# Performance work log

Measured on AMD Instinct MI355X. Metric: run time of the kernel, lower is better.

## Reference

```python
import jax, jax.numpy as jnp
import numpy as np
import math

B, N_SEQ, SEQ_LEN, C_M = 1, 256, 256, 256
N_HEADS, C_HIDDEN = 8, 32
HC = N_HEADS * C_HIDDEN
LN_EPS = 1e-5


def setup_inputs() -> dict:
    key = jax.random.key(0)
    ks = jax.random.split(key, 8)
    s_in = 1.0 / math.sqrt(C_M)
    s_out = 1.0 / math.sqrt(HC)
    return {
        "m": jax.random.normal(ks[0], (B, N_SEQ, SEQ_LEN, C_M), dtype=jnp.float32),
        "ln_w": jnp.ones((C_M,), dtype=jnp.float32),
        "ln_b": jnp.zeros((C_M,), dtype=jnp.float32),
        "wq": jax.random.normal(ks[1], (C_M, HC), dtype=jnp.float32) * s_in,
        "wk": jax.random.normal(ks[2], (C_M, HC), dtype=jnp.float32) * s_in,
        "wv": jax.random.normal(ks[3], (C_M, HC), dtype=jnp.float32) * s_in,
        "wg": jax.random.normal(ks[4], (C_M, HC), dtype=jnp.float32) * s_in,
        "bg": jnp.zeros((HC,), dtype=jnp.float32),
        "wo": jax.random.normal(ks[5], (HC, C_M), dtype=jnp.float32) * s_out,
        "bo": jnp.zeros((C_M,), dtype=jnp.float32),
    }


def reference(m, ln_w, ln_b, wq, wk, wv, wg, bg, wo, bo):
    b, s, l, _ = m.shape  # [B, n_seq, seq_len, c_m]
    # LayerNorm over c_m
    mu = jnp.mean(m, axis=-1, keepdims=True)
    var = jnp.mean(jnp.square(m - mu), axis=-1, keepdims=True)
    mn = (m - mu) * jax.lax.rsqrt(var + LN_EPS) * ln_w + ln_b  # [B, S, L, c_m]
    mt = jnp.swapaxes(mn, 1, 2)  # [B, L, S, c_m] -- attend over n_seq per column
    # QKV projections (no bias), split heads: [B, L, H, S, ch]
    def proj(w):
        return jnp.transpose(
            (mt @ w).reshape(b, l, s, N_HEADS, C_HIDDEN), (0, 1, 3, 2, 4)
        )
    q, k, v = proj(wq), proj(wk), proj(wv)
    logits = jnp.einsum("blhsc,blhtc->blhst", q, k) / math.sqrt(C_HIDDEN)
    weights = jax.nn.softmax(logits, axis=-1)
    o = jnp.einsum("blhst,blhtc->blhsc", weights, v)  # [B, L, H, S, ch]
    # Faithful to source: permute(0,2,1,3,4) -> [B, H, L, S, ch], then raw reshape
    o = jnp.transpose(o, (0, 2, 1, 3, 4))
    o = o.reshape(b, s, l, HC)  # data-scrambling reshape, as in source
    # Sigmoid gating on layer-normed input (m.transpose(1,2).transpose(1,2) == mn)
    g = jax.nn.sigmoid(mn @ wg + bg)  # [B, S, L, HC]
    o = g * o
    return o @ wo + bo  # [B, S, L, c_m]
```

## Files before the change

### kernel.cpp

```cpp
#include <hip/hip_runtime.h>

typedef unsigned short u16;
typedef __attribute__((ext_vector_type(8))) short bf16x8;
typedef __attribute__((ext_vector_type(4))) float f32x4;

__device__ __forceinline__ float b2f(u16 u){ return __uint_as_float(((unsigned int)u)<<16); }
__device__ __forceinline__ u16 f2b(float f){
  unsigned int u = __float_as_uint(f);
  u += 0x7fffu + ((u>>16)&1u);
  return (u16)(u>>16);
}

__global__ __launch_bounds__(256) void k_ln(const float* __restrict__ m,
    const float* __restrict__ lw, const float* __restrict__ lb,
    u16* __restrict__ mnb){
  int row = blockIdx.x*4 + (threadIdx.x>>6);
  int s = row>>8, l = row&255;
  int ln = threadIdx.x&63;
  float4 x = *(const float4*)(m + (size_t)row*256 + ln*4);
  float s1 = x.x+x.y+x.z+x.w;
  float s2 = x.x*x.x + x.y*x.y + x.z*x.z + x.w*x.w;
  #pragma unroll
  for (int off=32; off>0; off>>=1){
    s1 += __shfl_xor(s1, off);
    s2 += __shfl_xor(s2, off);
  }
  float mu  = s1*(1.0f/256.0f);
  float inv = rsqrtf(s2*(1.0f/256.0f) - mu*mu + 1e-5f);
  float4 w = *(const float4*)(lw + ln*4);
  float4 b = *(const float4*)(lb + ln*4);
  u16 o[4];
  o[0] = f2b((x.x-mu)*inv*w.x + b.x);
  o[1] = f2b((x.y-mu)*inv*w.y + b.y);
  o[2] = f2b((x.z-mu)*inv*w.z + b.z);
  o[3] = f2b((x.w-mu)*inv*w.w + b.w);
  *(ushort4*)(mnb + ((size_t)l*256 + s)*256 + ln*4) = *(ushort4*)o;
}

__global__ __launch_bounds__(256) void k_wprep(
    const float* __restrict__ wq, const float* __restrict__ wk,
    const float* __restrict__ wv, const float* __restrict__ wg,
    const float* __restrict__ wo, u16* __restrict__ WT){
  int n = blockIdx.x, z = blockIdx.y, tid = threadIdx.x;
  const float* W = (z==0)?wq:(z==1)?wk:(z==2)?wv:(z==3)?wg:wo;
  WT[(size_t)z*65536 + (size_t)n*256 + tid] = f2b(W[(size_t)tid*256 + n]);
}

__global__ __launch_bounds__(256,2) void k_fused(const u16* __restrict__ mnb,
    const u16* __restrict__ WT, const float* __restrict__ bg,
    const float* __restrict__ bo, float* __restrict__ outp){
  __shared__ u16 smem[39168];
  u16* QS = smem;
  u16* KS = smem + 10240;
  u16* VT = smem + 20480;
  u16* PB = smem + 28928;
  float* OS = (float*)smem;
  u16* GS = smem + 20480;

  int bx = blockIdx.x;
  int h = bx>>8, l = bx&255;
  int tid = threadIdx.x;
  int lane = tid&63, wid = tid>>6, quad = lane>>4, lo = lane&15;
  int m0 = wid*64;
  f32x4 z4 = {0.f,0.f,0.f,0.f};

  const u16* Abase = mnb + (size_t)l*65536;
  const u16* Bq = WT + (size_t)0*65536 + (size_t)h*32*256;
  const u16* Bk = WT + (size_t)1*65536 + (size_t)h*32*256;
  const u16* Bv = WT + (size_t)2*65536 + (size_t)h*32*256;
  f32x4 acc[4][6];
  #pragma unroll
  for (int a=0;a<4;++a)
    #pragma unroll
    for (int b=0;b<6;++b) acc[a][b]=z4;

  for (int ks=0; ks<8; ++ks){
    bf16x8 af[4];
    #pragma unroll
    for (int mt=0; mt<4; ++mt)
      af[mt] = *(const bf16x8*)(Abase + (size_t)(m0+mt*16+lo)*256 + ks*32 + quad*8);
    bf16x8 bq[2], bk2[2], bv2[2];
    #pragma unroll
    for (int c2=0; c2<2; ++c2){
      bq[c2]  = *(const bf16x8*)(Bq + (size_t)(c2*16+lo)*256 + ks*32 + quad*8);
      bk2[c2] = *(const bf16x8*)(Bk + (size_t)(c2*16+lo)*256 + ks*32 + quad*8);
      bv2[c2] = *(const bf16x8*)(Bv + (size_t)(c2*16+lo)*256 + ks*32 + quad*8);
    }
    #pragma unroll
    for (int mt=0; mt<4; ++mt){
      #pragma unroll
      for (int c2=0; c2<2; ++c2){
        acc[mt][0+c2] = __builtin_amdgcn_mfma_f32_16x16x32_bf16(af[mt], bq[c2],  acc[mt][0+c2], 0,0,0);
        acc[mt][2+c2] = __builtin_amdgcn_mfma_f32_16x16x32_bf16(af[mt], bk2[c2], acc[mt][2+c2], 0,0,0);
        acc[mt][4+c2] = __builtin_amdgcn_mfma_f32_16x16x32_bf16(af[mt], bv2[c2], acc[mt][4+c2], 0,0,0);
      }
    }
  }
  #pragma unroll
  for (int mt=0; mt<4; ++mt)
    #pragma unroll
    for (int ntl=0; ntl<2; ++ntl)
      #pragma unroll
      for (int r=0; r<4; ++r){
        int s = m0 + mt*16 + quad*4 + r;
        QS[s*40 + ntl*16+lo] = f2b(acc[mt][0+ntl][r]);
        KS[s*40 + ntl*16+lo] = f2b(acc[mt][2+ntl][r]);
        VT[(ntl*16+lo)*264 + s] = f2b(acc[mt][4+ntl][r]);
      }
  bf16x8 qf[4];
  #pragma unroll
  for (int mt=0; mt<4; ++mt)
    qf[mt] = *(const bf16x8*)&QS[(m0+mt*16+lo)*40 + quad*8];
  __syncthreads();

  const float scale = 0.17677669529663687f;
  float lr[16];
  #pragma unroll
  for (int i=0;i<16;++i) lr[i]=0.f;
  f32x4 o_acc[4][2];
  #pragma unroll
  for (int a=0;a<4;++a){ o_acc[a][0]=z4; o_acc[a][1]=z4; }
  int pbase = wid*64*40;

  for (int ts=0; ts<8; ++ts){
    bf16x8 kf[2];
    #pragma unroll
    for (int ntl=0; ntl<2; ++ntl)
      kf[ntl] = *(const bf16x8*)&KS[(ts*32+ntl*16+lo)*40 + quad*8];
    #pragma unroll
    for (int mt=0; mt<4; ++mt){
      #pragma unroll
      for (int ntl=0; ntl<2; ++ntl){
        f32x4 sa = __builtin_amdgcn_mfma_f32_16x16x32_bf16(qf[mt], kf[ntl], z4, 0,0,0);
        #pragma unroll
        for (int r=0; r<4; ++r){
          float p = __expf(sa[r]*scale);
          lr[mt*4+r] += p;
          PB[pbase + (mt*16+quad*4+r)*40 + ntl*16+lo] = f2b(p);
        }
      }
    }
    bf16x8 vf[2];
    #pragma unroll
    for (int nc=0; nc<2; ++nc)
      vf[nc] = *(const bf16x8*)&VT[(nc*16+lo)*264 + ts*32 + quad*8];
    #pragma unroll
    for (int mt=0; mt<4; ++mt){
      bf16x8 paf = *(const bf16x8*)&PB[pbase + (mt*16+lo)*40 + quad*8];
      #pragma unroll
      for (int nc=0; nc<2; ++nc)
        o_acc[mt][nc] = __builtin_amdgcn_mfma_f32_16x16x32_bf16(paf, vf[nc], o_acc[mt][nc], 0,0,0);
    }
  }
  #pragma unroll
  for (int i=0;i<16;++i){
    float v = lr[i];
    v += __shfl_xor(v, 1);
    v += __shfl_xor(v, 2);
    v += __shfl_xor(v, 4);
    v += __shfl_xor(v, 8);
    lr[i] = 1.0f / v;
  }
  __syncthreads();
  #pragma unroll
  for (int mt=0; mt<4; ++mt)
    #pragma unroll
    for (int nc=0; nc<2; ++nc)
      #pragma unroll
      for (int r=0; r<4; ++r){
        int s = m0 + mt*16 + quad*4 + r;
        int c = nc*16 + lo;
        OS[s*32 + c] = o_acc[mt][nc][r] * lr[mt*4+r];
      }
  __syncthreads();

  int sp  = h*32 + (l>>3);
  int l0p = (l&7)*32;
  int wn0 = wid*64;
  const u16* Gw = WT + (size_t)3*65536;
  f32x4 gacc[2][4];
  #pragma unroll
  for (int a=0;a<2;++a)
    #pragma unroll
    for (int b=0;b<4;++b) gacc[a][b]=z4;
  for (int ks=0; ks<8; ++ks){
    bf16x8 ga[2];
    #pragma unroll
    for (int mt2=0; mt2<2; ++mt2)
      ga[mt2] = *(const bf16x8*)(mnb + ((size_t)(l0p+mt2*16+lo)*256 + sp)*256 + ks*32 + quad*8);
    bf16x8 gb[4];
    #pragma unroll
    for (int nt=0; nt<4; ++nt)
      gb[nt] = *(const bf16x8*)(Gw + (size_t)(wn0+nt*16+lo)*256 + ks*32 + quad*8);
    #pragma unroll
    for (int mt2=0; mt2<2; ++mt2)
      #pragma unroll
      for (int nt=0; nt<4; ++nt)
        gacc[mt2][nt] = __builtin_amdgcn_mfma_f32_16x16x32_bf16(ga[mt2], gb[nt], gacc[mt2][nt], 0,0,0);
  }
  #pragma unroll
  for (int nt=0; nt<4; ++nt){
    int n = wn0 + nt*16 + lo;
    float bgn = bg[n];
    #pragma unroll
    for (int mt2=0; mt2<2; ++mt2)
      #pragma unroll
      for (int r=0; r<4; ++r){
        int j = mt2*16 + quad*4 + r;
        float g = 1.f/(1.f + __expf(-(gacc[mt2][nt][r] + bgn)));
        GS[j*264 + n] = f2b(g * OS[j*256 + n]);
      }
  }
  __syncthreads();

  const u16* Ow = WT + (size_t)4*65536;
  f32x4 pacc[2][4];
  #pragma unroll
  for (int a=0;a<2;++a)
    #pragma unroll
    for (int b=0;b<4;++b) pacc[a][b]=z4;
  for (int ks=0; ks<8; ++ks){
    bf16x8 pa[2];
    #pragma unroll
    for (int mt2=0; mt2<2; ++mt2)
      pa[mt2] = *(const bf16x8*)&GS[(mt2*16+lo)*264 + ks*32 + quad*8];
    bf16x8 pb[4];
    #pragma unroll
    for (int nt=0; nt<4; ++nt)
      pb[nt] = *(const bf16x8*)(Ow + (size_t)(wn0+nt*16+lo)*256 + ks*32 + quad*8);
    #pragma unroll
    for (int mt2=0; mt2<2; ++mt2)
      #pragma unroll
      for (int nt=0; nt<4; ++nt)
        pacc[mt2][nt] = __builtin_amdgcn_mfma_f32_16x16x32_bf16(pa[mt2], pb[nt], pacc[mt2][nt], 0,0,0);
  }
  #pragma unroll
  for (int nt=0; nt<4; ++nt){
    int n = wn0 + nt*16 + lo;
    float bon = bo[n];
    #pragma unroll
    for (int mt2=0; mt2<2; ++mt2)
      #pragma unroll
      for (int r=0; r<4; ++r){
        int j = mt2*16 + quad*4 + r;
        outp[((size_t)sp*256 + l0p + j)*256 + n] = pacc[mt2][nt][r] + bon;
      }
  }
}

extern "C" void kernel_launch(void* const* d_in, const int* in_sizes, int n_in,
                              void* d_out, int out_size, void* d_ws, size_t ws_size,
                              hipStream_t stream){
  const float* m  = (const float*)d_in[0];
  const float* lw = (const float*)d_in[1];
  const float* lb = (const float*)d_in[2];
  const float* wq = (const float*)d_in[3];
  const float* wk = (const float*)d_in[4];
  const float* wv = (const float*)d_in[5];
  const float* wg = (const float*)d_in[6];
  const float* bg = (const float*)d_in[7];
  const float* wo = (const float*)d_in[8];
  const float* bo = (const float*)d_in[9];

  u16* mnb = (u16*)d_ws;
  u16* WT  = mnb + (size_t)16777216;
  float* out = (float*)d_out;

  k_wprep<<<dim3(256,5), 256, 0, stream>>>(wq, wk, wv, wg, wo, WT);
  k_ln   <<<16384,       256, 0, stream>>>(m, lw, lb, mnb);
  k_fused<<<2048,        256, 0, stream>>>(mnb, WT, bg, bo, out);
}
```

Before: 296.6 us.

## Shrink fused-kernel LDS for 3 blocks/CU, remap blocks for XCD locality, coalesce prep kernels

The fused attention kernel's shared memory drops from about 78KB to about 54KB by aliasing the P buffer onto the Q region, which is already loaded into registers, and by packing K rows at stride 32. Launch bounds rise to 3 blocks per CU. Block indices are remapped so the 8 heads of one column l run on the same XCD, which is meant to improve L2 reuse of the normalized input. The LayerNorm kernel now handles 8 rows per wave with a smaller grid, and the weight transpose stages through LDS to get coalesced writes. The unpadded K stride may add LDS bank conflicts, and the higher occupancy could raise register pressure.

```diff
diff --git a/kernel.cpp b/kernel.cpp
--- a/kernel.cpp
+++ b/kernel.cpp
@@ -14,51 +14,69 @@
 __global__ __launch_bounds__(256) void k_ln(const float* __restrict__ m,
     const float* __restrict__ lw, const float* __restrict__ lb,
     u16* __restrict__ mnb){
-  int row = blockIdx.x*4 + (threadIdx.x>>6);
-  int s = row>>8, l = row&255;
+  int bx = blockIdx.x;
+  int l = bx>>3;
+  int s0 = (bx&7)*32 + (threadIdx.x>>6)*8;
   int ln = threadIdx.x&63;
-  float4 x = *(const float4*)(m + (size_t)row*256 + ln*4);
-  float s1 = x.x+x.y+x.z+x.w;
-  float s2 = x.x*x.x + x.y*x.y + x.z*x.z + x.w*x.w;
-  #pragma unroll
-  for (int off=32; off>0; off>>=1){
-    s1 += __shfl_xor(s1, off);
-    s2 += __shfl_xor(s2, off);
-  }
-  float mu  = s1*(1.0f/256.0f);
-  float inv = rsqrtf(s2*(1.0f/256.0f) - mu*mu + 1e-5f);
   float4 w = *(const float4*)(lw + ln*4);
   float4 b = *(const float4*)(lb + ln*4);
-  u16 o[4];
-  o[0] = f2b((x.x-mu)*inv*w.x + b.x);
-  o[1] = f2b((x.y-mu)*inv*w.y + b.y);
-  o[2] = f2b((x.z-mu)*inv*w.z + b.z);
-  o[3] = f2b((x.w-mu)*inv*w.w + b.w);
-  *(ushort4*)(mnb + ((size_t)l*256 + s)*256 + ln*4) = *(ushort4*)o;
+  #pragma unroll
+  for (int i=0;i<8;++i){
+    int s = s0 + i;
+    float4 x = *(const float4*)(m + ((size_t)s*256 + l)*256 + ln*4);
+    float s1 = x.x+x.y+x.z+x.w;
+    float s2 = x.x*x.x + x.y*x.y + x.z*x.z + x.w*x.w;
+    #pragma unroll
+    for (int off=32; off>0; off>>=1){
+      s1 += __shfl_xor(s1, off);
+      s2 += __shfl_xor(s2, off);
+    }
+    float mu  = s1*(1.0f/256.0f);
+    float inv = rsqrtf(s2*(1.0f/256.0f) - mu*mu + 1e-5f);
+    u16 o[4];
+    o[0] = f2b((x.x-mu)*inv*w.x + b.x);
+    o[1] = f2b((x.y-mu)*inv*w.y + b.y);
+    o[2] = f2b((x.z-mu)*inv*w.z + b.z);
+    o[3] = f2b((x.w-mu)*inv*w.w + b.w);
+    *(ushort4*)(mnb + ((size_t)l*256 + s)*256 + ln*4) = *(ushort4*)o;
+  }
 }
 
 __global__ __launch_bounds__(256) void k_wprep(
     const float* __restrict__ wq, const float* __restrict__ wk,
     const float* __restrict__ wv, const float* __restrict__ wg,
     const float* __restrict__ wo, u16* __restrict__ WT){
-  int n = blockIdx.x, z = blockIdx.y, tid = threadIdx.x;
+  __shared__ u16 T[16*264];
+  int z = blockIdx.y, n0 = blockIdx.x*16, tid = threadIdx.x;
   const float* W = (z==0)?wq:(z==1)?wk:(z==2)?wv:(z==3)?wg:wo;
-  WT[(size_t)z*65536 + (size_t)n*256 + tid] = f2b(W[(size_t)tid*256 + n]);
-}
-
-__global__ __launch_bounds__(256,2) void k_fused(const u16* __restrict__ mnb,
+  int nl = tid&15;
+  #pragma unroll
+  for (int i=0;i<16;++i){
+    int cm = i*16 + (tid>>4);
+    T[nl*264 + cm] = f2b(W[(size_t)cm*256 + n0 + nl]);
+  }
+  __syncthreads();
+  int n = tid>>4, cc = (tid&15)*16;
+  uint4 a = *(const uint4*)&T[n*264 + cc];
+  uint4 c = *(const uint4*)&T[n*264 + cc + 8];
+  *(uint4*)&WT[(size_t)z*65536 + (size_t)(n0+n)*256 + cc]     = a;
+  *(uint4*)&WT[(size_t)z*65536 + (size_t)(n0+n)*256 + cc + 8] = c;
+}
+
+__global__ __launch_bounds__(256,3) void k_fused(const u16* __restrict__ mnb,
     const u16* __restrict__ WT, const float* __restrict__ bg,
     const float* __restrict__ bo, float* __restrict__ outp){
-  __shared__ u16 smem[39168];
+  __shared__ u16 smem[26880];
   u16* QS = smem;
   u16* KS = smem + 10240;
-  u16* VT = smem + 20480;
-  u16* PB = smem + 28928;
+  u16* VT = smem + 18432;
+  u16* PB = smem;
   float* OS = (float*)smem;
-  u16* GS = smem + 20480;
+  u16* GS = smem + 18432;
 
   int bx = blockIdx.x;
-  int h = bx>>8, l = bx&255;
+  int l = ((bx&7)<<5) | (bx>>6);
+  int h = (bx>>3)&7;
   int tid = threadIdx.x;
   int lane = tid&63, wid = tid>>6, quad = lane>>4, lo = lane&15;
   int m0 = wid*64;
@@ -104,7 +122,7 @@
       for (int r=0; r<4; ++r){
         int s = m0 + mt*16 + quad*4 + r;
         QS[s*40 + ntl*16+lo] = f2b(acc[mt][0+ntl][r]);
-        KS[s*40 + ntl*16+lo] = f2b(acc[mt][2+ntl][r]);
+        KS[s*32 + ntl*16+lo] = f2b(acc[mt][2+ntl][r]);
         VT[(ntl*16+lo)*264 + s] = f2b(acc[mt][4+ntl][r]);
       }
   bf16x8 qf[4];
@@ -126,7 +144,7 @@
     bf16x8 kf[2];
     #pragma unroll
     for (int ntl=0; ntl<2; ++ntl)
-      kf[ntl] = *(const bf16x8*)&KS[(ts*32+ntl*16+lo)*40 + quad*8];
+      kf[ntl] = *(const bf16x8*)&KS[(ts*32+ntl*16+lo)*32 + quad*8];
     #pragma unroll
     for (int mt=0; mt<4; ++mt){
       #pragma unroll
@@ -266,7 +284,7 @@
   u16* WT  = mnb + (size_t)16777216;
   float* out = (float*)d_out;
 
-  k_wprep<<<dim3(256,5), 256, 0, stream>>>(wq, wk, wv, wg, wo, WT);
-  k_ln   <<<16384,       256, 0, stream>>>(m, lw, lb, mnb);
-  k_fused<<<2048,        256, 0, stream>>>(mnb, WT, bg, bo, out);
-}
+  k_wprep<<<dim3(16,5), 256, 0, stream>>>(wq, wk, wv, wg, wo, WT);
+  k_ln   <<<2048,       256, 0, stream>>>(m, lw, lb, mnb);
+  k_fused<<<2048,       256, 0, stream>>>(mnb, WT, bg, bo, out);
+}
```

Result: faster. 283.5 us (-4.4%).
